# Optimization experiments

Measured on AMD Instinct MI355X. Metric: run time of the kernel, lower is better.

Reference implementation:

```python
import jax, jax.numpy as jnp
import numpy as np

SOS = 1
EOS = 2
M = 32  # max_y_seq_len


def gru_cell(x, h, W_ih, W_hh, b_ih, b_hh):
    # torch GRUCell math: gates ordered [r, z, n]
    gi = x @ W_ih.T + b_ih          # [B, 3H]
    gh = h @ W_hh.T + b_hh          # [B, 3H]
    i_r, i_z, i_n = jnp.split(gi, 3, axis=-1)
    h_r, h_z, h_n = jnp.split(gh, 3, axis=-1)
    r = jax.nn.sigmoid(i_r + h_r)
    z = jax.nn.sigmoid(i_z + h_z)
    n = jnp.tanh(i_n + r * h_n)
    return (1.0 - z) * n + z * h


def setup_inputs() -> dict:
    key = jax.random.key(0)
    ks = jax.random.split(key, 12)
    B, H, V = 256, 512, 16000
    s = 0.05  # keep GRU pre-activations in a sane range
    return {
        "sem_f": jax.random.normal(ks[0], (B, H), jnp.float32),
        "emb": jax.random.normal(ks[1], (V, H), jnp.float32) * 0.01,
        "W_ih0": jax.random.normal(ks[2], (3 * H, H), jnp.float32) * s,
        "W_hh0": jax.random.normal(ks[3], (3 * H, H), jnp.float32) * s,
        "b_ih0": jax.random.normal(ks[4], (3 * H,), jnp.float32) * s,
        "b_hh0": jax.random.normal(ks[5], (3 * H,), jnp.float32) * s,
        "W_ih1": jax.random.normal(ks[6], (3 * H, H), jnp.float32) * s,
        "W_hh1": jax.random.normal(ks[7], (3 * H, H), jnp.float32) * s,
        "b_ih1": jax.random.normal(ks[8], (3 * H,), jnp.float32) * s,
        "b_hh1": jax.random.normal(ks[9], (3 * H,), jnp.float32) * s,
        "fc_W": jax.random.normal(ks[10], (V, H), jnp.float32) * s,
        "fc_b": jax.random.normal(ks[11], (V,), jnp.float32) * s,
    }


def reference(sem_f, emb, W_ih0, W_hh0, b_ih0, b_hh0,
              W_ih1, W_hh1, b_ih1, b_hh1, fc_W, fc_b):
    B = sem_f.shape[0]
    # hidden = sem_f repeated for each GRU layer
    h0 = sem_f
    h1 = sem_f
    inputs = jnp.full((B,), SOS, dtype=jnp.int32)
    finished = jnp.zeros((B,), dtype=bool)

    def step(carry, _):
        inputs, h0, h1, finished = carry
        unf = ~finished                         # rows still active this step
        x = emb[inputs]                         # [B, H]
        h0n = gru_cell(x, h0, W_ih0, W_hh0, b_ih0, b_hh0)
        h1n = gru_cell(h0n, h1, W_ih1, W_hh1, b_ih1, b_hh1)
        out = h1n @ fc_W.T + fc_b               # [B, V]
        dec = jnp.argmax(out, axis=1).astype(jnp.int32)
        # emulate unf_idxs advanced-indexing writes: finished rows keep -1 / 0
        decoded_t = jnp.where(unf, dec, -1)
        logits_t = jnp.where(unf[:, None], out, 0.0)
        new_finished = finished | (unf & (dec == EOS))
        # pruned (finished) rows freeze hidden and inputs
        h0 = jnp.where(unf[:, None], h0n, h0)
        h1 = jnp.where(unf[:, None], h1n, h1)
        inputs = jnp.where(unf, dec, inputs)
        return (inputs, h0, h1, new_finished), (decoded_t, logits_t)

    _, (decoded, logits) = jax.lax.scan(step, (inputs, h0, h1, finished),
                                        None, length=M)
    decoded = decoded.T                          # [B, M]
    logits = jnp.transpose(logits, (1, 0, 2))    # [B, M, V]
    mask = decoded != -1
    return decoded, logits, mask
```

## Files before the change

### kernel.cpp

```cpp
#include <hip/hip_runtime.h>
#include <math.h>

#define B_   256
#define H_   512
#define V_   16000
#define M_   32
#define SOS_ 1
#define EOS_ 2
#define INV_SCALE (1.0f/2048.0f)

typedef _Float16 half_t;
typedef _Float16 f16x8 __attribute__((ext_vector_type(8)));
typedef _Float16 f16x4 __attribute__((ext_vector_type(4)));
typedef float    f32x4 __attribute__((ext_vector_type(4)));

__device__ __forceinline__ void split_f32(float x, half_t& a, half_t& b) {
    a = (half_t)x;
    b = (half_t)((x - (float)a) * 2048.0f);
}

__global__ __launch_bounds__(256)
void split_weights(const float* __restrict__ src, half_t* __restrict__ hi,
                   half_t* __restrict__ lo, int n4)
{
    const int i = blockIdx.x * 256 + threadIdx.x;
    if (i >= n4) return;
    const float4 v = ((const float4*)src)[i];
    f16x4 a, b;
    half_t t0, t1;
    split_f32(v.x, t0, t1); a[0] = t0; b[0] = t1;
    split_f32(v.y, t0, t1); a[1] = t0; b[1] = t1;
    split_f32(v.z, t0, t1); a[2] = t0; b[2] = t1;
    split_f32(v.w, t0, t1); a[3] = t0; b[3] = t1;
    ((f16x4*)hi)[i] = a;
    ((f16x4*)lo)[i] = b;
}

__global__ __launch_bounds__(256)
void init_kernel(const float* __restrict__ sem_f, const float* __restrict__ emb,
                 float* __restrict__ h0, float* __restrict__ h1,
                 half_t* __restrict__ h0a, half_t* __restrict__ h0b,
                 half_t* __restrict__ h1a, half_t* __restrict__ h1b,
                 half_t* __restrict__ xa,  half_t* __restrict__ xb,
                 int* __restrict__ inputs, int* __restrict__ finished)
{
    const int i = blockIdx.x * 256 + threadIdx.x;
    if (i < B_ * H_) {
        const float v = sem_f[i];
        h0[i] = v; h1[i] = v;
        half_t a, b; split_f32(v, a, b);
        h0a[i] = a; h0b[i] = b;
        h1a[i] = a; h1b[i] = b;
        const int j = i & (H_ - 1);
        const float xv = emb[SOS_ * H_ + j];
        half_t c, d; split_f32(xv, c, d);
        xa[i] = c; xb[i] = d;
    }
    if (i < B_) { inputs[i] = SOS_; finished[i] = 0; }
}

__global__ __launch_bounds__(256)
void gru_gemm_mfma(const half_t* __restrict__ Aia, const half_t* __restrict__ Aib,
                   const half_t* __restrict__ Aha, const half_t* __restrict__ Ahb,
                   const half_t* __restrict__ Wia, const half_t* __restrict__ Wib,
                   const half_t* __restrict__ Wha, const half_t* __restrict__ Whb,
                   const float* __restrict__ b_ih, const float* __restrict__ b_hh,
                   float* __restrict__ PRE)
{
    const int ct = blockIdx.x;
    const int rt = blockIdx.y;
    const bool is_ih = (ct < 12);
    const int wrow0 = (is_ih ? ct : ct - 12) * 128;
    const int row0  = rt * 32;
    const float*  bias = is_ih ? b_ih : b_hh;
    const half_t* Aa   = is_ih ? Aia : Aha;
    const half_t* Ab   = is_ih ? Aib : Ahb;
    const half_t* W0   = is_ih ? Wia : Wha;
    const half_t* W1   = is_ih ? Wib : Whb;

    __shared__ half_t W0s[128][40];
    __shared__ half_t W1s[128][40];

    const int tid  = threadIdx.x;
    const int w    = tid >> 6;
    const int lane = tid & 63;
    const int ll   = lane & 15;
    const int lg   = lane >> 4;

    const int sc = tid >> 1;
    const int sk = (tid & 1) * 16;
    const half_t* wp0 = W0 + (size_t)(wrow0 + sc) * H_ + sk;
    const half_t* wp1 = W1 + (size_t)(wrow0 + sc) * H_ + sk;

    f32x4 accM[2][2] = {};
    f32x4 accC[2][2] = {};

    for (int k0 = 0; k0 < H_; k0 += 32) {
        const f16x8 s0 = *(const f16x8*)(wp0 + k0);
        const f16x8 s1 = *(const f16x8*)(wp0 + k0 + 8);
        const f16x8 s2 = *(const f16x8*)(wp1 + k0);
        const f16x8 s3 = *(const f16x8*)(wp1 + k0 + 8);
        __syncthreads();
        *(f16x8*)&W0s[sc][sk]     = s0;
        *(f16x8*)&W0s[sc][sk + 8] = s1;
        *(f16x8*)&W1s[sc][sk]     = s2;
        *(f16x8*)&W1s[sc][sk + 8] = s3;
        __syncthreads();

        f16x8 a0[2], a1[2];
#pragma unroll
        for (int rf = 0; rf < 2; ++rf) {
            const size_t off = ((size_t)(row0 + 16*rf + ll) << 9) + k0 + (lg << 3);
            a0[rf] = *(const f16x8*)(Aa + off);
            a1[rf] = *(const f16x8*)(Ab + off);
        }
#pragma unroll
        for (int cf = 0; cf < 2; ++cf) {
            const int c = 32*w + 16*cf + ll;
            const f16x8 b0 = *(const f16x8*)&W0s[c][lg << 3];
            const f16x8 b1 = *(const f16x8*)&W1s[c][lg << 3];
#pragma unroll
            for (int rf = 0; rf < 2; ++rf) {
                accM[rf][cf] = __builtin_amdgcn_mfma_f32_16x16x32_f16(a0[rf], b0, accM[rf][cf], 0,0,0);
                accC[rf][cf] = __builtin_amdgcn_mfma_f32_16x16x32_f16(a0[rf], b1, accC[rf][cf], 0,0,0);
                accC[rf][cf] = __builtin_amdgcn_mfma_f32_16x16x32_f16(a1[rf], b0, accC[rf][cf], 0,0,0);
            }
        }
    }

#pragma unroll
    for (int cf = 0; cf < 2; ++cf) {
        const int cl = 32*w + 16*cf + ll;
        const float bv = bias[wrow0 + cl];
        const int c = ct * 128 + cl;
#pragma unroll
        for (int rf = 0; rf < 2; ++rf) {
#pragma unroll
            for (int r = 0; r < 4; ++r) {
                const int row = row0 + 16*rf + lg*4 + r;
                PRE[(size_t)row * 3072 + c] = accM[rf][cf][r] + accC[rf][cf][r] * INV_SCALE + bv;
            }
        }
    }
}

__global__ __launch_bounds__(256)
void gate_kernel(const float* __restrict__ PRE,
                 float* __restrict__ h,
                 half_t* __restrict__ ha, half_t* __restrict__ hb,
                 const int* __restrict__ finished)
{
    const int idx = blockIdx.x * 256 + threadIdx.x;
    const int b = idx >> 9;
    const int j = idx & 511;
    if (finished[b]) return;
    const float* p = PRE + (size_t)b * 3072;
    const float ir = p[j],        iz = p[512 + j],  in_ = p[1024 + j];
    const float hr = p[1536 + j], hz = p[2048 + j], hn  = p[2560 + j];
    const float r = 1.0f / (1.0f + expf(-(ir + hr)));
    const float z = 1.0f / (1.0f + expf(-(iz + hz)));
    const float n = tanhf(in_ + r * hn);
    const float hv = (1.0f - z) * n + z * h[idx];
    h[idx] = hv;
    half_t a, bb; split_f32(hv, a, bb);
    ha[idx] = a; hb[idx] = bb;
}

__global__ __launch_bounds__(256)
void fc_gemm_mfma(const half_t* __restrict__ Aa, const half_t* __restrict__ Ab,
                  const half_t* __restrict__ W0, const half_t* __restrict__ W1,
                  const float* __restrict__ fcb,
                  const int* __restrict__ finished,
                  float* __restrict__ logits,
                  float* __restrict__ pmax, int* __restrict__ pidx, int t)
{
    const int ct = blockIdx.x;
    const int rt = blockIdx.y;
    const int col0 = ct * 128;
    const int row0 = rt * 64;

    __shared__ half_t W0s[128][40];
    __shared__ half_t W1s[128][40];
    __shared__ float  pmS[64][2];
    __shared__ int    piS[64][2];

    const int tid  = threadIdx.x;
    const int wv   = tid >> 6;
    const int wr   = wv >> 1, wc = wv & 1;
    const int lane = tid & 63;
    const int ll   = lane & 15, lg = lane >> 4;

    const int sc = tid >> 1;
    const int sk = (tid & 1) * 16;
    const half_t* wp0 = W0 + (size_t)(col0 + sc) * H_ + sk;
    const half_t* wp1 = W1 + (size_t)(col0 + sc) * H_ + sk;

    f32x4 accM[2][4] = {};
    f32x4 accC[2][4] = {};

    for (int k0 = 0; k0 < H_; k0 += 32) {
        const f16x8 s0 = *(const f16x8*)(wp0 + k0);
        const f16x8 s1 = *(const f16x8*)(wp0 + k0 + 8);
        const f16x8 s2 = *(const f16x8*)(wp1 + k0);
        const f16x8 s3 = *(const f16x8*)(wp1 + k0 + 8);
        __syncthreads();
        *(f16x8*)&W0s[sc][sk]     = s0;
        *(f16x8*)&W0s[sc][sk + 8] = s1;
        *(f16x8*)&W1s[sc][sk]     = s2;
        *(f16x8*)&W1s[sc][sk + 8] = s3;
        __syncthreads();

        f16x8 a0[2], a1[2];
#pragma unroll
        for (int rf = 0; rf < 2; ++rf) {
            const size_t off = ((size_t)(row0 + 32*wr + 16*rf + ll) << 9) + k0 + (lg << 3);
            a0[rf] = *(const f16x8*)(Aa + off);
            a1[rf] = *(const f16x8*)(Ab + off);
        }
#pragma unroll
        for (int cf = 0; cf < 4; ++cf) {
            const int c = 64*wc + 16*cf + ll;
            const f16x8 b0 = *(const f16x8*)&W0s[c][lg << 3];
            const f16x8 b1 = *(const f16x8*)&W1s[c][lg << 3];
#pragma unroll
            for (int rf = 0; rf < 2; ++rf) {
                accM[rf][cf] = __builtin_amdgcn_mfma_f32_16x16x32_f16(a0[rf], b0, accM[rf][cf], 0,0,0);
                accC[rf][cf] = __builtin_amdgcn_mfma_f32_16x16x32_f16(a0[rf], b1, accC[rf][cf], 0,0,0);
                accC[rf][cf] = __builtin_amdgcn_mfma_f32_16x16x32_f16(a1[rf], b0, accC[rf][cf], 0,0,0);
            }
        }
    }

    int fin[2][4];
#pragma unroll
    for (int rf = 0; rf < 2; ++rf)
#pragma unroll
        for (int r = 0; r < 4; ++r)
            fin[rf][r] = finished[row0 + 32*wr + 16*rf + lg*4 + r];

    float bvv[2][4];
    int   bii[2][4];
#pragma unroll
    for (int rf = 0; rf < 2; ++rf)
#pragma unroll
        for (int r = 0; r < 4; ++r) { bvv[rf][r] = -INFINITY; bii[rf][r] = 0x7fffffff; }

#pragma unroll
    for (int cf = 0; cf < 4; ++cf) {
        const int col = col0 + 64*wc + 16*cf + ll;
        const float bv = fcb[col];
#pragma unroll
        for (int rf = 0; rf < 2; ++rf) {
#pragma unroll
            for (int r = 0; r < 4; ++r) {
                const int row = row0 + 32*wr + 16*rf + lg*4 + r;
                const float raw = accM[rf][cf][r] + accC[rf][cf][r] * INV_SCALE + bv;
                logits[((size_t)row * M_ + t) * V_ + col] = fin[rf][r] ? 0.0f : raw;
                if (raw > bvv[rf][r]) { bvv[rf][r] = raw; bii[rf][r] = col; }
            }
        }
    }

#pragma unroll
    for (int rf = 0; rf < 2; ++rf) {
#pragma unroll
        for (int r = 0; r < 4; ++r) {
            float v = bvv[rf][r]; int ix = bii[rf][r];
#pragma unroll
            for (int m = 1; m < 16; m <<= 1) {
                const float ov = __shfl_xor(v, m);
                const int   oi = __shfl_xor(ix, m);
                if (ov > v || (ov == v && oi < ix)) { v = ov; ix = oi; }
            }
            if (ll == 0) {
                const int lr = 32*wr + 16*rf + lg*4 + r;
                pmS[lr][wc] = v; piS[lr][wc] = ix;
            }
        }
    }
    __syncthreads();
    if (tid < 64) {
        float v = pmS[tid][0]; int ix = piS[tid][0];
        const float v2 = pmS[tid][1]; const int i2 = piS[tid][1];
        if (v2 > v || (v2 == v && i2 < ix)) { v = v2; ix = i2; }
        pmax[(row0 + tid) * 128 + ct] = v;
        pidx[(row0 + tid) * 128 + ct] = ix;
    }
}

__global__ __launch_bounds__(128)
void finalize_kernel(const float* __restrict__ pmax, const int* __restrict__ pidx,
                     const float* __restrict__ emb,
                     int* __restrict__ inputs, int* __restrict__ finished,
                     float* __restrict__ decoded_out, float* __restrict__ mask_out,
                     half_t* __restrict__ xa, half_t* __restrict__ xb, int t)
{
    const int b = blockIdx.x;
    const int tid = threadIdx.x;
    __shared__ float sv[128];
    __shared__ int   si[128];
    float v = -INFINITY; int ix = 0x7fffffff;
    if (tid < 125) { v = pmax[b * 128 + tid]; ix = pidx[b * 128 + tid]; }
    sv[tid] = v; si[tid] = ix;
    __syncthreads();
    for (int s = 64; s > 0; s >>= 1) {
        if (tid < s) {
            const float v2 = sv[tid + s]; const int i2 = si[tid + s];
            if (v2 > sv[tid] || (v2 == sv[tid] && i2 < si[tid])) { sv[tid] = v2; si[tid] = i2; }
        }
        __syncthreads();
    }
    __shared__ int s_tok;
    if (tid == 0) {
        const int fin = finished[b];
        const int dec = si[0];
        decoded_out[b * M_ + t] = fin ? -1.0f : (float)dec;
        mask_out   [b * M_ + t] = fin ? 0.0f : 1.0f;
        int tok;
        if (!fin) { inputs[b] = dec; if (dec == EOS_) finished[b] = 1; tok = dec; }
        else tok = inputs[b];
        s_tok = tok;
    }
    __syncthreads();
    const int tok = s_tok;
    for (int j = tid; j < H_; j += 128) {
        const float v2 = emb[(size_t)tok * H_ + j];
        half_t a, bb; split_f32(v2, a, bb);
        xa[b * H_ + j] = a; xb[b * H_ + j] = bb;
    }
}

extern "C" void kernel_launch(void* const* d_in, const int* in_sizes, int n_in,
                              void* d_out, int out_size, void* d_ws, size_t ws_size,
                              hipStream_t stream)
{
    const float* sem_f = (const float*)d_in[0];
    const float* emb   = (const float*)d_in[1];
    const float* W_ih0 = (const float*)d_in[2];
    const float* W_hh0 = (const float*)d_in[3];
    const float* b_ih0 = (const float*)d_in[4];
    const float* b_hh0 = (const float*)d_in[5];
    const float* W_ih1 = (const float*)d_in[6];
    const float* W_hh1 = (const float*)d_in[7];
    const float* b_ih1 = (const float*)d_in[8];
    const float* b_hh1 = (const float*)d_in[9];
    const float* fc_W  = (const float*)d_in[10];
    const float* fc_b  = (const float*)d_in[11];

    float* out = (float*)d_out;
    float* decoded_out = out;
    float* logits_out  = out + (size_t)B_ * M_;
    float* mask_out    = out + (size_t)B_ * M_ + (size_t)B_ * M_ * V_;

    float*  ws  = (float*)d_ws;
    float*  PRE = ws;
    float*  h0  = ws + 786432;
    float*  h1  = ws + 917504;
    half_t* h0a = (half_t*)(ws + 1048576);
    half_t* h0b = (half_t*)(ws + 1114112);
    half_t* h1a = (half_t*)(ws + 1179648);
    half_t* h1b = (half_t*)(ws + 1245184);
    half_t* xa  = (half_t*)(ws + 1310720);
    half_t* xb  = (half_t*)(ws + 1376256);
    float*  pmax = ws + 1441792;
    int*    pidx = (int*)(ws + 1474560);
    int*    inputs   = (int*)(ws + 1507328);
    int*    finished = (int*)(ws + 1507584);
    half_t* wi0a = (half_t*)(ws + 1507840);
    half_t* wi0b = (half_t*)(ws + 1901056);
    half_t* wh0a = (half_t*)(ws + 2294272);
    half_t* wh0b = (half_t*)(ws + 2687488);
    half_t* wi1a = (half_t*)(ws + 3080704);
    half_t* wi1b = (half_t*)(ws + 3473920);
    half_t* wh1a = (half_t*)(ws + 3867136);
    half_t* wh1b = (half_t*)(ws + 4260352);
    half_t* fca  = (half_t*)(ws + 4653568);
    half_t* fcbp = (half_t*)(ws + 8749568);

    const int nGru4 = (1536 * 512) / 4;
    const int nFc4  = (V_ * H_) / 4;
    split_weights<<<(nGru4 + 255) / 256, 256, 0, stream>>>(W_ih0, wi0a, wi0b, nGru4);
    split_weights<<<(nGru4 + 255) / 256, 256, 0, stream>>>(W_hh0, wh0a, wh0b, nGru4);
    split_weights<<<(nGru4 + 255) / 256, 256, 0, stream>>>(W_ih1, wi1a, wi1b, nGru4);
    split_weights<<<(nGru4 + 255) / 256, 256, 0, stream>>>(W_hh1, wh1a, wh1b, nGru4);
    split_weights<<<(nFc4 + 255) / 256, 256, 0, stream>>>(fc_W, fca, fcbp, nFc4);

    init_kernel<<<(B_ * H_ + 255) / 256, 256, 0, stream>>>(
        sem_f, emb, h0, h1, h0a, h0b, h1a, h1b, xa, xb, inputs, finished);

    const dim3 gruGrid(24, 8);
    const dim3 fcGrid(125, 4);

    for (int t = 0; t < M_; ++t) {
        gru_gemm_mfma<<<gruGrid, 256, 0, stream>>>(
            xa, xb, h0a, h0b, wi0a, wi0b, wh0a, wh0b, b_ih0, b_hh0, PRE);
        gate_kernel<<<(B_ * H_) / 256, 256, 0, stream>>>(PRE, h0, h0a, h0b, finished);
        gru_gemm_mfma<<<gruGrid, 256, 0, stream>>>(
            h0a, h0b, h1a, h1b, wi1a, wi1b, wh1a, wh1b, b_ih1, b_hh1, PRE);
        gate_kernel<<<(B_ * H_) / 256, 256, 0, stream>>>(PRE, h1, h1a, h1b, finished);
        fc_gemm_mfma<<<fcGrid, 256, 0, stream>>>(
            h1a, h1b, fca, fcbp, fc_b, finished, logits_out, pmax, pidx, t);
        finalize_kernel<<<B_, 128, 0, stream>>>(
            pmax, pidx, emb, inputs, finished, decoded_out, mask_out, xa, xb, t);
    }
}
```

Baseline: 2.979 ms.

## Fuse whole decode loop into one persistent cooperative kernel with grid syncs

Replaces the per-step chain of six kernel launches over 32 steps with a single cooperative persistent kernel. It does the weight splitting, init, both GRU layers, gates, FC and argmax finalize in one launch, separated by grid-wide barriers. GEMM tiles are also reshaped to 64 weight columns by 128 rows, so each block reuses its loaded weight tile across more batch rows. This removes launch overhead and inter-kernel gaps, at the cost of grid-sync latency and a fixed block count. A non-cooperative fallback path is kept.

```diff
diff --git a/kernel.cpp b/kernel.cpp
--- a/kernel.cpp
+++ b/kernel.cpp
@@ -1,5 +1,8 @@
 #include <hip/hip_runtime.h>
+#include <hip/hip_cooperative_groups.h>
 #include <math.h>
+
+namespace cg = cooperative_groups;
 
 #define B_   256
 #define H_   512
@@ -8,119 +11,97 @@
 #define SOS_ 1
 #define EOS_ 2
 #define INV_SCALE (1.0f/2048.0f)
+#define NTHR 256
 
 typedef _Float16 half_t;
 typedef _Float16 f16x8 __attribute__((ext_vector_type(8)));
 typedef _Float16 f16x4 __attribute__((ext_vector_type(4)));
 typedef float    f32x4 __attribute__((ext_vector_type(4)));
 
+struct Params {
+    const float *sem_f, *emb;
+    const float *b_ih0, *b_hh0, *b_ih1, *b_hh1, *fc_b;
+    const float *W_ih0, *W_hh0, *W_ih1, *W_hh1, *fc_W;
+    float *decoded, *logits, *mask;
+    float *PRE, *h0, *h1;
+    half_t *h0a, *h0b, *h1a, *h1b, *xa, *xb;
+    float *pmax; int *pidx; int *inputs; int *finished;
+    half_t *wi0a, *wi0b, *wh0a, *wh0b, *wi1a, *wi1b, *wh1a, *wh1b, *fca, *fcbp;
+};
+
 __device__ __forceinline__ void split_f32(float x, half_t& a, half_t& b) {
     a = (half_t)x;
     b = (half_t)((x - (float)a) * 2048.0f);
 }
 
-__global__ __launch_bounds__(256)
-void split_weights(const float* __restrict__ src, half_t* __restrict__ hi,
-                   half_t* __restrict__ lo, int n4)
-{
-    const int i = blockIdx.x * 256 + threadIdx.x;
-    if (i >= n4) return;
-    const float4 v = ((const float4*)src)[i];
-    f16x4 a, b;
-    half_t t0, t1;
-    split_f32(v.x, t0, t1); a[0] = t0; b[0] = t1;
-    split_f32(v.y, t0, t1); a[1] = t0; b[1] = t1;
-    split_f32(v.z, t0, t1); a[2] = t0; b[2] = t1;
-    split_f32(v.w, t0, t1); a[3] = t0; b[3] = t1;
-    ((f16x4*)hi)[i] = a;
-    ((f16x4*)lo)[i] = b;
-}
-
-__global__ __launch_bounds__(256)
-void init_kernel(const float* __restrict__ sem_f, const float* __restrict__ emb,
-                 float* __restrict__ h0, float* __restrict__ h1,
-                 half_t* __restrict__ h0a, half_t* __restrict__ h0b,
-                 half_t* __restrict__ h1a, half_t* __restrict__ h1b,
-                 half_t* __restrict__ xa,  half_t* __restrict__ xb,
-                 int* __restrict__ inputs, int* __restrict__ finished)
-{
-    const int i = blockIdx.x * 256 + threadIdx.x;
-    if (i < B_ * H_) {
-        const float v = sem_f[i];
-        h0[i] = v; h1[i] = v;
-        half_t a, b; split_f32(v, a, b);
-        h0a[i] = a; h0b[i] = b;
-        h1a[i] = a; h1b[i] = b;
-        const int j = i & (H_ - 1);
-        const float xv = emb[SOS_ * H_ + j];
-        half_t c, d; split_f32(xv, c, d);
-        xa[i] = c; xb[i] = d;
-    }
-    if (i < B_) { inputs[i] = SOS_; finished[i] = 0; }
-}
-
-__global__ __launch_bounds__(256)
-void gru_gemm_mfma(const half_t* __restrict__ Aia, const half_t* __restrict__ Aib,
-                   const half_t* __restrict__ Aha, const half_t* __restrict__ Ahb,
-                   const half_t* __restrict__ Wia, const half_t* __restrict__ Wib,
-                   const half_t* __restrict__ Wha, const half_t* __restrict__ Whb,
-                   const float* __restrict__ b_ih, const float* __restrict__ b_hh,
-                   float* __restrict__ PRE)
-{
-    const int ct = blockIdx.x;
-    const int rt = blockIdx.y;
-    const bool is_ih = (ct < 12);
-    const int wrow0 = (is_ih ? ct : ct - 12) * 128;
-    const int row0  = rt * 32;
+__device__ __forceinline__ void split_plane_dev(const float* __restrict__ src,
+    half_t* __restrict__ hi, half_t* __restrict__ lo, int n4, int gidx, int gst)
+{
+    for (int i = gidx; i < n4; i += gst) {
+        const float4 v = ((const float4*)src)[i];
+        f16x4 a, b; half_t t0, t1;
+        split_f32(v.x, t0, t1); a[0] = t0; b[0] = t1;
+        split_f32(v.y, t0, t1); a[1] = t0; b[1] = t1;
+        split_f32(v.z, t0, t1); a[2] = t0; b[2] = t1;
+        split_f32(v.w, t0, t1); a[3] = t0; b[3] = t1;
+        ((f16x4*)hi)[i] = a; ((f16x4*)lo)[i] = b;
+    }
+}
+
+
+__device__ void gru_tile(int ct, int rt,
+    const half_t* __restrict__ Aia, const half_t* __restrict__ Aib,
+    const half_t* __restrict__ Aha, const half_t* __restrict__ Ahb,
+    const half_t* __restrict__ Wia, const half_t* __restrict__ Wib,
+    const half_t* __restrict__ Wha, const half_t* __restrict__ Whb,
+    const float* __restrict__ b_ih, const float* __restrict__ b_hh,
+    float* __restrict__ PRE,
+    half_t (*W0s)[40], half_t (*W1s)[40])
+{
+    const bool is_ih = (ct < 24);
+    const int wrow0 = (is_ih ? ct : ct - 24) * 64;
+    const int row0  = rt * 128;
     const float*  bias = is_ih ? b_ih : b_hh;
-    const half_t* Aa   = is_ih ? Aia : Aha;
-    const half_t* Ab   = is_ih ? Aib : Ahb;
-    const half_t* W0   = is_ih ? Wia : Wha;
-    const half_t* W1   = is_ih ? Wib : Whb;
-
-    __shared__ half_t W0s[128][40];
-    __shared__ half_t W1s[128][40];
+    const half_t* Aa = is_ih ? Aia : Aha;
+    const half_t* Ab = is_ih ? Aib : Ahb;
+    const half_t* W0 = is_ih ? Wia : Wha;
+    const half_t* W1 = is_ih ? Wib : Whb;
 
     const int tid  = threadIdx.x;
-    const int w    = tid >> 6;
+    const int wv   = tid >> 6;
+    const int wr   = wv >> 1, wc = wv & 1;
     const int lane = tid & 63;
-    const int ll   = lane & 15;
-    const int lg   = lane >> 4;
-
-    const int sc = tid >> 1;
-    const int sk = (tid & 1) * 16;
+    const int ll   = lane & 15, lg = lane >> 4;
+    const int sc   = tid >> 2;
+    const int sk   = (tid & 3) * 8;
     const half_t* wp0 = W0 + (size_t)(wrow0 + sc) * H_ + sk;
     const half_t* wp1 = W1 + (size_t)(wrow0 + sc) * H_ + sk;
 
-    f32x4 accM[2][2] = {};
-    f32x4 accC[2][2] = {};
+    f32x4 accM[4][2] = {};
+    f32x4 accC[4][2] = {};
 
     for (int k0 = 0; k0 < H_; k0 += 32) {
         const f16x8 s0 = *(const f16x8*)(wp0 + k0);
-        const f16x8 s1 = *(const f16x8*)(wp0 + k0 + 8);
-        const f16x8 s2 = *(const f16x8*)(wp1 + k0);
-        const f16x8 s3 = *(const f16x8*)(wp1 + k0 + 8);
+        const f16x8 s1 = *(const f16x8*)(wp1 + k0);
         __syncthreads();
-        *(f16x8*)&W0s[sc][sk]     = s0;
-        *(f16x8*)&W0s[sc][sk + 8] = s1;
-        *(f16x8*)&W1s[sc][sk]     = s2;
-        *(f16x8*)&W1s[sc][sk + 8] = s3;
+        *(f16x8*)&W0s[sc][sk] = s0;
+        *(f16x8*)&W1s[sc][sk] = s1;
         __syncthreads();
 
-        f16x8 a0[2], a1[2];
-#pragma unroll
-        for (int rf = 0; rf < 2; ++rf) {
-            const size_t off = ((size_t)(row0 + 16*rf + ll) << 9) + k0 + (lg << 3);
+        f16x8 a0[4], a1[4];
+#pragma unroll
+        for (int rf = 0; rf < 4; ++rf) {
+            const size_t off = ((size_t)(row0 + 64*wr + 16*rf + ll) << 9) + k0 + (lg << 3);
             a0[rf] = *(const f16x8*)(Aa + off);
             a1[rf] = *(const f16x8*)(Ab + off);
         }
 #pragma unroll
         for (int cf = 0; cf < 2; ++cf) {
-            const int c = 32*w + 16*cf + ll;
+            const int c = 32*wc + 16*cf + ll;
             const f16x8 b0 = *(const f16x8*)&W0s[c][lg << 3];
             const f16x8 b1 = *(const f16x8*)&W1s[c][lg << 3];
 #pragma unroll
-            for (int rf = 0; rf < 2; ++rf) {
+            for (int rf = 0; rf < 4; ++rf) {
                 accM[rf][cf] = __builtin_amdgcn_mfma_f32_16x16x32_f16(a0[rf], b0, accM[rf][cf], 0,0,0);
                 accC[rf][cf] = __builtin_amdgcn_mfma_f32_16x16x32_f16(a0[rf], b1, accC[rf][cf], 0,0,0);
                 accC[rf][cf] = __builtin_amdgcn_mfma_f32_16x16x32_f16(a1[rf], b0, accC[rf][cf], 0,0,0);
@@ -130,27 +111,130 @@
 
 #pragma unroll
     for (int cf = 0; cf < 2; ++cf) {
-        const int cl = 32*w + 16*cf + ll;
+        const int cl = 32*wc + 16*cf + ll;
         const float bv = bias[wrow0 + cl];
-        const int c = ct * 128 + cl;
-#pragma unroll
-        for (int rf = 0; rf < 2; ++rf) {
+        const int c = ct * 64 + cl;
+#pragma unroll
+        for (int rf = 0; rf < 4; ++rf) {
 #pragma unroll
             for (int r = 0; r < 4; ++r) {
-                const int row = row0 + 16*rf + lg*4 + r;
+                const int row = row0 + 64*wr + 16*rf + lg*4 + r;
                 PRE[(size_t)row * 3072 + c] = accM[rf][cf][r] + accC[rf][cf][r] * INV_SCALE + bv;
             }
         }
     }
 }
 
-__global__ __launch_bounds__(256)
-void gate_kernel(const float* __restrict__ PRE,
-                 float* __restrict__ h,
-                 half_t* __restrict__ ha, half_t* __restrict__ hb,
-                 const int* __restrict__ finished)
-{
-    const int idx = blockIdx.x * 256 + threadIdx.x;
+__device__ void fc_tile(int ct, int rt,
+    const half_t* __restrict__ Aa, const half_t* __restrict__ Ab,
+    const half_t* __restrict__ W0, const half_t* __restrict__ W1,
+    const float* __restrict__ fcb, const int* __restrict__ finished,
+    float* __restrict__ logits, float* __restrict__ pmax, int* __restrict__ pidx,
+    int t, half_t (*W0s)[40], half_t (*W1s)[40], float (*pmS)[2], int (*piS)[2])
+{
+    const int col0 = ct * 64;
+    const int row0 = rt * 128;
+    const int tid  = threadIdx.x;
+    const int wv   = tid >> 6;
+    const int wr   = wv >> 1, wc = wv & 1;
+    const int lane = tid & 63;
+    const int ll   = lane & 15, lg = lane >> 4;
+    const int sc   = tid >> 2;
+    const int sk   = (tid & 3) * 8;
+    const half_t* wp0 = W0 + (size_t)(col0 + sc) * H_ + sk;
+    const half_t* wp1 = W1 + (size_t)(col0 + sc) * H_ + sk;
+
+    f32x4 accM[4][2] = {};
+    f32x4 accC[4][2] = {};
+
+    for (int k0 = 0; k0 < H_; k0 += 32) {
+        const f16x8 s0 = *(const f16x8*)(wp0 + k0);
+        const f16x8 s1 = *(const f16x8*)(wp1 + k0);
+        __syncthreads();
+        *(f16x8*)&W0s[sc][sk] = s0;
+        *(f16x8*)&W1s[sc][sk] = s1;
+        __syncthreads();
+
+        f16x8 a0[4], a1[4];
+#pragma unroll
+        for (int rf = 0; rf < 4; ++rf) {
+            const size_t off = ((size_t)(row0 + 64*wr + 16*rf + ll) << 9) + k0 + (lg << 3);
+            a0[rf] = *(const f16x8*)(Aa + off);
+            a1[rf] = *(const f16x8*)(Ab + off);
+        }
+#pragma unroll
+        for (int cf = 0; cf < 2; ++cf) {
+            const int c = 32*wc + 16*cf + ll;
+            const f16x8 b0 = *(const f16x8*)&W0s[c][lg << 3];
+            const f16x8 b1 = *(const f16x8*)&W1s[c][lg << 3];
+#pragma unroll
+            for (int rf = 0; rf < 4; ++rf) {
+                accM[rf][cf] = __builtin_amdgcn_mfma_f32_16x16x32_f16(a0[rf], b0, accM[rf][cf], 0,0,0);
+                accC[rf][cf] = __builtin_amdgcn_mfma_f32_16x16x32_f16(a0[rf], b1, accC[rf][cf], 0,0,0);
+                accC[rf][cf] = __builtin_amdgcn_mfma_f32_16x16x32_f16(a1[rf], b0, accC[rf][cf], 0,0,0);
+            }
+        }
+    }
+
+    int fin[4][4];
+    float bvv[4][4];
+    int   bii[4][4];
+#pragma unroll
+    for (int rf = 0; rf < 4; ++rf)
+#pragma unroll
+        for (int r = 0; r < 4; ++r) {
+            fin[rf][r] = finished[row0 + 64*wr + 16*rf + lg*4 + r];
+            bvv[rf][r] = -INFINITY; bii[rf][r] = 0x7fffffff;
+        }
+
+#pragma unroll
+    for (int cf = 0; cf < 2; ++cf) {
+        const int col = col0 + 32*wc + 16*cf + ll;
+        const float bv = fcb[col];
+#pragma unroll
+        for (int rf = 0; rf < 4; ++rf) {
+#pragma unroll
+            for (int r = 0; r < 4; ++r) {
+                const int row = row0 + 64*wr + 16*rf + lg*4 + r;
+                const float raw = accM[rf][cf][r] + accC[rf][cf][r] * INV_SCALE + bv;
+                logits[((size_t)row * M_ + t) * V_ + col] = fin[rf][r] ? 0.0f : raw;
+                if (raw > bvv[rf][r]) { bvv[rf][r] = raw; bii[rf][r] = col; }
+            }
+        }
+    }
+
+#pragma unroll
+    for (int rf = 0; rf < 4; ++rf) {
+#pragma unroll
+        for (int r = 0; r < 4; ++r) {
+            float v = bvv[rf][r]; int ix = bii[rf][r];
+#pragma unroll
+            for (int m = 1; m < 16; m <<= 1) {
+                const float ov = __shfl_xor(v, m);
+                const int   oi = __shfl_xor(ix, m);
+                if (ov > v || (ov == v && oi < ix)) { v = ov; ix = oi; }
+            }
+            if (ll == 0) {
+                const int lr = 64*wr + 16*rf + lg*4 + r;
+                pmS[lr][wc] = v; piS[lr][wc] = ix;
+            }
+        }
+    }
+    __syncthreads();
+    if (tid < 128) {
+        float v = pmS[tid][0]; int ix = piS[tid][0];
+        const float v2 = pmS[tid][1]; const int i2 = piS[tid][1];
+        if (v2 > v || (v2 == v && i2 < ix)) { v = v2; ix = i2; }
+        pmax[(size_t)(row0 + tid) * 256 + ct] = v;
+        pidx[(size_t)(row0 + tid) * 256 + ct] = ix;
+    }
+    __syncthreads();
+}
+
+__device__ __forceinline__ void gate_elem(const float* __restrict__ PRE,
+    float* __restrict__ h, half_t* __restrict__ ha, half_t* __restrict__ hb,
+    const int* __restrict__ finished, int idx)
+{
     const int b = idx >> 9;
     const int j = idx & 511;
     if (finished[b]) return;
@@ -166,241 +250,254 @@
     ha[idx] = a; hb[idx] = bb;
 }
 
-__global__ __launch_bounds__(256)
-void fc_gemm_mfma(const half_t* __restrict__ Aa, const half_t* __restrict__ Ab,
-                  const half_t* __restrict__ W0, const half_t* __restrict__ W1,
-                  const float* __restrict__ fcb,
-                  const int* __restrict__ finished,
-                  float* __restrict__ logits,
-                  float* __restrict__ pmax, int* __restrict__ pidx, int t)
-{
-    const int ct = blockIdx.x;
-    const int rt = blockIdx.y;
-    const int col0 = ct * 128;
-    const int row0 = rt * 64;
-
-    __shared__ half_t W0s[128][40];
-    __shared__ half_t W1s[128][40];
-    __shared__ float  pmS[64][2];
-    __shared__ int    piS[64][2];
-
-    const int tid  = threadIdx.x;
-    const int wv   = tid >> 6;
-    const int wr   = wv >> 1, wc = wv & 1;
-    const int lane = tid & 63;
-    const int ll   = lane & 15, lg = lane >> 4;
-
-    const int sc = tid >> 1;
-    const int sk = (tid & 1) * 16;
-    const half_t* wp0 = W0 + (size_t)(col0 + sc) * H_ + sk;
-    const half_t* wp1 = W1 + (size_t)(col0 + sc) * H_ + sk;
-
-    f32x4 accM[2][4] = {};
-    f32x4 accC[2][4] = {};
-
-    for (int k0 = 0; k0 < H_; k0 += 32) {
-        const f16x8 s0 = *(const f16x8*)(wp0 + k0);
-        const f16x8 s1 = *(const f16x8*)(wp0 + k0 + 8);
-        const f16x8 s2 = *(const f16x8*)(wp1 + k0);
-        const f16x8 s3 = *(const f16x8*)(wp1 + k0 + 8);
-        __syncthreads();
-        *(f16x8*)&W0s[sc][sk]     = s0;
-        *(f16x8*)&W0s[sc][sk + 8] = s1;
-        *(f16x8*)&W1s[sc][sk]     = s2;
-        *(f16x8*)&W1s[sc][sk + 8] = s3;
-        __syncthreads();
-
-        f16x8 a0[2], a1[2];
-#pragma unroll
-        for (int rf = 0; rf < 2; ++rf) {
-            const size_t off = ((size_t)(row0 + 32*wr + 16*rf + ll) << 9) + k0 + (lg << 3);
-            a0[rf] = *(const f16x8*)(Aa + off);
-            a1[rf] = *(const f16x8*)(Ab + off);
-        }
-#pragma unroll
-        for (int cf = 0; cf < 4; ++cf) {
-            const int c = 64*wc + 16*cf + ll;
-            const f16x8 b0 = *(const f16x8*)&W0s[c][lg << 3];
-            const f16x8 b1 = *(const f16x8*)&W1s[c][lg << 3];
-#pragma unroll
-            for (int rf = 0; rf < 2; ++rf) {
-                accM[rf][cf] = __builtin_amdgcn_mfma_f32_16x16x32_f16(a0[rf], b0, accM[rf][cf], 0,0,0);
-                accC[rf][cf] = __builtin_amdgcn_mfma_f32_16x16x32_f16(a0[rf], b1, accC[rf][cf], 0,0,0);
-                accC[rf][cf] = __builtin_amdgcn_mfma_f32_16x16x32_f16(a1[rf], b0, accC[rf][cf], 0,0,0);
-            }
-        }
-    }
-
-    int fin[2][4];
-#pragma unroll
-    for (int rf = 0; rf < 2; ++rf)
-#pragma unroll
-        for (int r = 0; r < 4; ++r)
-            fin[rf][r] = finished[row0 + 32*wr + 16*rf + lg*4 + r];
-
-    float bvv[2][4];
-    int   bii[2][4];
-#pragma unroll
-    for (int rf = 0; rf < 2; ++rf)
-#pragma unroll
-        for (int r = 0; r < 4; ++r) { bvv[rf][r] = -INFINITY; bii[rf][r] = 0x7fffffff; }
-
-#pragma unroll
-    for (int cf = 0; cf < 4; ++cf) {
-        const int col = col0 + 64*wc + 16*cf + ll;
-        const float bv = fcb[col];
-#pragma unroll
-        for (int rf = 0; rf < 2; ++rf) {
-#pragma unroll
-            for (int r = 0; r < 4; ++r) {
-                const int row = row0 + 32*wr + 16*rf + lg*4 + r;
-                const float raw = accM[rf][cf][r] + accC[rf][cf][r] * INV_SCALE + bv;
-                logits[((size_t)row * M_ + t) * V_ + col] = fin[rf][r] ? 0.0f : raw;
-                if (raw > bvv[rf][r]) { bvv[rf][r] = raw; bii[rf][r] = col; }
-            }
-        }
-    }
-
-#pragma unroll
-    for (int rf = 0; rf < 2; ++rf) {
-#pragma unroll
-        for (int r = 0; r < 4; ++r) {
-            float v = bvv[rf][r]; int ix = bii[rf][r];
-#pragma unroll
-            for (int m = 1; m < 16; m <<= 1) {
-                const float ov = __shfl_xor(v, m);
-                const int   oi = __shfl_xor(ix, m);
-                if (ov > v || (ov == v && oi < ix)) { v = ov; ix = oi; }
-            }
-            if (ll == 0) {
-                const int lr = 32*wr + 16*rf + lg*4 + r;
-                pmS[lr][wc] = v; piS[lr][wc] = ix;
-            }
-        }
-    }
-    __syncthreads();
-    if (tid < 64) {
-        float v = pmS[tid][0]; int ix = piS[tid][0];
-        const float v2 = pmS[tid][1]; const int i2 = piS[tid][1];
-        if (v2 > v || (v2 == v && i2 < ix)) { v = v2; ix = i2; }
-        pmax[(row0 + tid) * 128 + ct] = v;
-        pidx[(row0 + tid) * 128 + ct] = ix;
-    }
-}
-
-__global__ __launch_bounds__(128)
-void finalize_kernel(const float* __restrict__ pmax, const int* __restrict__ pidx,
-                     const float* __restrict__ emb,
-                     int* __restrict__ inputs, int* __restrict__ finished,
-                     float* __restrict__ decoded_out, float* __restrict__ mask_out,
-                     half_t* __restrict__ xa, half_t* __restrict__ xb, int t)
-{
-    const int b = blockIdx.x;
+__device__ void finalize_row(int b, const Params& p, int t,
+                             float* sv, int* si, int* s_tok)
+{
     const int tid = threadIdx.x;
-    __shared__ float sv[128];
-    __shared__ int   si[128];
     float v = -INFINITY; int ix = 0x7fffffff;
-    if (tid < 125) { v = pmax[b * 128 + tid]; ix = pidx[b * 128 + tid]; }
+    if (tid < 250) { v = p.pmax[(size_t)b * 256 + tid]; ix = p.pidx[(size_t)b * 256 + tid]; }
     sv[tid] = v; si[tid] = ix;
     __syncthreads();
-    for (int s = 64; s > 0; s >>= 1) {
+    for (int s = 128; s > 0; s >>= 1) {
         if (tid < s) {
             const float v2 = sv[tid + s]; const int i2 = si[tid + s];
             if (v2 > sv[tid] || (v2 == sv[tid] && i2 < si[tid])) { sv[tid] = v2; si[tid] = i2; }
         }
         __syncthreads();
     }
-    __shared__ int s_tok;
     if (tid == 0) {
-        const int fin = finished[b];
+        const int fin = p.finished[b];
         const int dec = si[0];
-        decoded_out[b * M_ + t] = fin ? -1.0f : (float)dec;
-        mask_out   [b * M_ + t] = fin ? 0.0f : 1.0f;
+        p.decoded[b * M_ + t] = fin ? -1.0f : (float)dec;
+        p.mask   [b * M_ + t] = fin ? 0.0f : 1.0f;
         int tok;
-        if (!fin) { inputs[b] = dec; if (dec == EOS_) finished[b] = 1; tok = dec; }
-        else tok = inputs[b];
-        s_tok = tok;
+        if (!fin) { p.inputs[b] = dec; if (dec == EOS_) p.finished[b] = 1; tok = dec; }
+        else tok = p.inputs[b];
+        *s_tok = tok;
     }
     __syncthreads();
-    const int tok = s_tok;
-    for (int j = tid; j < H_; j += 128) {
-        const float v2 = emb[(size_t)tok * H_ + j];
+    const int tok = *s_tok;
+    for (int j = tid; j < H_; j += NTHR) {
+        const float v2 = p.emb[(size_t)tok * H_ + j];
         half_t a, bb; split_f32(v2, a, bb);
-        xa[b * H_ + j] = a; xb[b * H_ + j] = bb;
-    }
+        p.xa[b * H_ + j] = a; p.xb[b * H_ + j] = bb;
+    }
+    __syncthreads();
+}
+
+__global__ __launch_bounds__(NTHR, 2)
+void scan_coop(Params p)
+{
+    cg::grid_group grid = cg::this_grid();
+
+    __shared__ half_t W0s[64][40];
+    __shared__ half_t W1s[64][40];
+    __shared__ float  red_f[256];
+    __shared__ int    red_i[256];
+    __shared__ int    s_tok;
+
+    const int nblk = gridDim.x;
+    const int blk  = blockIdx.x;
+    const int tid  = threadIdx.x;
+    const int gidx = blk * NTHR + tid;
+    const int gst  = nblk * NTHR;
+
+    split_plane_dev(p.W_ih0, p.wi0a, p.wi0b, (1536*512)/4, gidx, gst);
+    split_plane_dev(p.W_hh0, p.wh0a, p.wh0b, (1536*512)/4, gidx, gst);
+    split_plane_dev(p.W_ih1, p.wi1a, p.wi1b, (1536*512)/4, gidx, gst);
+    split_plane_dev(p.W_hh1, p.wh1a, p.wh1b, (1536*512)/4, gidx, gst);
+    split_plane_dev(p.fc_W,  p.fca,  p.fcbp, (V_*H_)/4,    gidx, gst);
+    for (int i = gidx; i < B_ * H_; i += gst) {
+        const float v = p.sem_f[i];
+        p.h0[i] = v; p.h1[i] = v;
+        half_t a, b; split_f32(v, a, b);
+        p.h0a[i] = a; p.h0b[i] = b;
+        p.h1a[i] = a; p.h1b[i] = b;
+        const int j = i & (H_ - 1);
+        const float xv = p.emb[SOS_ * H_ + j];
+        half_t c, d; split_f32(xv, c, d);
+        p.xa[i] = c; p.xb[i] = d;
+    }
+    for (int i = gidx; i < B_; i += gst) { p.inputs[i] = SOS_; p.finished[i] = 0; }
+    grid.sync();
+
+    for (int t = 0; t < M_; ++t) {
+        for (int tile = blk; tile < 96; tile += nblk)
+            gru_tile(tile % 48, tile / 48, p.xa, p.xb, p.h0a, p.h0b,
+                     p.wi0a, p.wi0b, p.wh0a, p.wh0b, p.b_ih0, p.b_hh0, p.PRE, W0s, W1s);
+        grid.sync();
+        for (int i = gidx; i < B_ * H_; i += gst)
+            gate_elem(p.PRE, p.h0, p.h0a, p.h0b, p.finished, i);
+        grid.sync();
+        for (int tile = blk; tile < 96; tile += nblk)
+            gru_tile(tile % 48, tile / 48, p.h0a, p.h0b, p.h1a, p.h1b,
+                     p.wi1a, p.wi1b, p.wh1a, p.wh1b, p.b_ih1, p.b_hh1, p.PRE, W0s, W1s);
+        grid.sync();
+        for (int i = gidx; i < B_ * H_; i += gst)
+            gate_elem(p.PRE, p.h1, p.h1a, p.h1b, p.finished, i);
+        grid.sync();
+        for (int tile = blk; tile < 500; tile += nblk)
+            fc_tile(tile % 250, tile / 250, p.h1a, p.h1b, p.fca, p.fcbp, p.fc_b,
+                    p.finished, p.logits, p.pmax, p.pidx, t, W0s, W1s,
+                    (float(*)[2])red_f, (int(*)[2])red_i);
+        grid.sync();
+        for (int b = blk; b < B_; b += nblk)
+            finalize_row(b, p, t, red_f, red_i, &s_tok);
+        grid.sync();
+    }
+}
+
+__global__ __launch_bounds__(256)
+void split_weights_k(const float* __restrict__ src, half_t* __restrict__ hi,
+                     half_t* __restrict__ lo, int n4)
+{
+    const int i = blockIdx.x * 256 + threadIdx.x;
+    if (i >= n4) return;
+    const float4 v = ((const float4*)src)[i];
+    f16x4 a, b; half_t t0, t1;
+    split_f32(v.x, t0, t1); a[0] = t0; b[0] = t1;
+    split_f32(v.y, t0, t1); a[1] = t0; b[1] = t1;
+    split_f32(v.z, t0, t1); a[2] = t0; b[2] = t1;
+    split_f32(v.w, t0, t1); a[3] = t0; b[3] = t1;
+    ((f16x4*)hi)[i] = a; ((f16x4*)lo)[i] = b;
+}
+
+__global__ __launch_bounds__(256)
+void init_k(Params p)
+{
+    const int i = blockIdx.x * 256 + threadIdx.x;
+    if (i < B_ * H_) {
+        const float v = p.sem_f[i];
+        p.h0[i] = v; p.h1[i] = v;
+        half_t a, b; split_f32(v, a, b);
+        p.h0a[i] = a; p.h0b[i] = b;
+        p.h1a[i] = a; p.h1b[i] = b;
+        const int j = i & (H_ - 1);
+        const float xv = p.emb[SOS_ * H_ + j];
+        half_t c, d; split_f32(xv, c, d);
+        p.xa[i] = c; p.xb[i] = d;
+    }
+    if (i < B_) { p.inputs[i] = SOS_; p.finished[i] = 0; }
+}
+
+__global__ __launch_bounds__(256)
+void gru_k(const half_t* Aia, const half_t* Aib, const half_t* Aha, const half_t* Ahb,
+           const half_t* Wia, const half_t* Wib, const half_t* Wha, const half_t* Whb,
+           const float* b_ih, const float* b_hh, float* PRE)
+{
+    __shared__ half_t W0s[64][40];
+    __shared__ half_t W1s[64][40];
+    gru_tile(blockIdx.x, blockIdx.y, Aia, Aib, Aha, Ahb,
+             Wia, Wib, Wha, Whb, b_ih, b_hh, PRE, W0s, W1s);
+}
+
+__global__ __launch_bounds__(256)
+void gate_k(const float* PRE, float* h, half_t* ha, half_t* hb, const int* finished)
+{
+    gate_elem(PRE, h, ha, hb, finished, blockIdx.x * 256 + threadIdx.x);
+}
+
+__global__ __launch_bounds__(256)
+void fc_k(const half_t* Aa, const half_t* Ab, const half_t* W0, const half_t* W1,
+          const float* fcb, const int* finished, float* logits,
+          float* pmax, int* pidx, int t)
+{
+    __shared__ half_t W0s[64][40];
+    __shared__ half_t W1s[64][40];
+    __shared__ float  pmS[128][2];
+    __shared__ int    piS[128][2];
+    fc_tile(blockIdx.x, blockIdx.y, Aa, Ab, W0, W1, fcb, finished,
+            logits, pmax, pidx, t, W0s, W1s, pmS, piS);
+}
+
+__global__ __launch_bounds__(256)
+void finalize_k(Params p, int t)
+{
+    __shared__ float sv[256];
+    __shared__ int   si[256];
+    __shared__ int   s_tok;
+    finalize_row(blockIdx.x, p, t, sv, si, &s_tok);
 }
 
 extern "C" void kernel_launch(void* const* d_in, const int* in_sizes, int n_in,
                               void* d_out, int out_size, void* d_ws, size_t ws_size,
                               hipStream_t stream)
 {
-    const float* sem_f = (const float*)d_in[0];
-    const float* emb   = (const float*)d_in[1];
-    const float* W_ih0 = (const float*)d_in[2];
-    const float* W_hh0 = (const float*)d_in[3];
-    const float* b_ih0 = (const float*)d_in[4];
-    const float* b_hh0 = (const float*)d_in[5];
-    const float* W_ih1 = (const float*)d_in[6];
-    const float* W_hh1 = (const float*)d_in[7];
-    const float* b_ih1 = (const float*)d_in[8];
-    const float* b_hh1 = (const float*)d_in[9];
-    const float* fc_W  = (const float*)d_in[10];
-    const float* fc_b  = (const float*)d_in[11];
+    Params p;
+    p.sem_f = (const float*)d_in[0];
+    p.emb   = (const float*)d_in[1];
+    p.W_ih0 = (const float*)d_in[2];
+    p.W_hh0 = (const float*)d_in[3];
+    p.b_ih0 = (const float*)d_in[4];
+    p.b_hh0 = (const float*)d_in[5];
+    p.W_ih1 = (const float*)d_in[6];
+    p.W_hh1 = (const float*)d_in[7];
+    p.b_ih1 = (const float*)d_in[8];
+    p.b_hh1 = (const float*)d_in[9];
+    p.fc_W  = (const float*)d_in[10];
+    p.fc_b  = (const float*)d_in[11];
 
     float* out = (float*)d_out;
-    float* decoded_out = out;
-    float* logits_out  = out + (size_t)B_ * M_;
-    float* mask_out    = out + (size_t)B_ * M_ + (size_t)B_ * M_ * V_;
-
-    float*  ws  = (float*)d_ws;
-    float*  PRE = ws;
-    float*  h0  = ws + 786432;
-    float*  h1  = ws + 917504;
-    half_t* h0a = (half_t*)(ws + 1048576);
-    half_t* h0b = (half_t*)(ws + 1114112);
-    half_t* h1a = (half_t*)(ws + 1179648);
-    half_t* h1b = (half_t*)(ws + 1245184);
-    half_t* xa  = (half_t*)(ws + 1310720);
-    half_t* xb  = (half_t*)(ws + 1376256);
-    float*  pmax = ws + 1441792;
-    int*    pidx = (int*)(ws + 1474560);
-    int*    inputs   = (int*)(ws + 1507328);
-    int*    finished = (int*)(ws + 1507584);
-    half_t* wi0a = (half_t*)(ws + 1507840);
-    half_t* wi0b = (half_t*)(ws + 1901056);
-    half_t* wh0a = (half_t*)(ws + 2294272);
-    half_t* wh0b = (half_t*)(ws + 2687488);
-    half_t* wi1a = (half_t*)(ws + 3080704);
-    half_t* wi1b = (half_t*)(ws + 3473920);
-    half_t* wh1a = (half_t*)(ws + 3867136);
-    half_t* wh1b = (half_t*)(ws + 4260352);
-    half_t* fca  = (half_t*)(ws + 4653568);
-    half_t* fcbp = (half_t*)(ws + 8749568);
+    p.decoded = out;
+    p.logits  = out + (size_t)B_ * M_;
+    p.mask    = out + (size_t)B_ * M_ + (size_t)B_ * M_ * V_;
+
+    float* ws = (float*)d_ws;
+    p.PRE  = ws;
+    p.h0   = ws + 786432;
+    p.h1   = ws + 917504;
+    p.h0a  = (half_t*)(ws + 1048576);
+    p.h0b  = (half_t*)(ws + 1114112);
+    p.h1a  = (half_t*)(ws + 1179648);
+    p.h1b  = (half_t*)(ws + 1245184);
+    p.xa   = (half_t*)(ws + 1310720);
+    p.xb   = (half_t*)(ws + 1376256);
+    p.pmax = ws + 1441792;
+    p.pidx = (int*)(ws + 1507328);
+    p.inputs   = (int*)(ws + 1572864);
+    p.finished = (int*)(ws + 1573120);
+    p.wi0a = (half_t*)(ws + 1573376);
+    p.wi0b = (half_t*)(ws + 1966592);
+    p.wh0a = (half_t*)(ws + 2359808);
+    p.wh0b = (half_t*)(ws + 2753024);
+    p.wi1a = (half_t*)(ws + 3146240);
+    p.wi1b = (half_t*)(ws + 3539456);
+    p.wh1a = (half_t*)(ws + 3932672);
+    p.wh1b = (half_t*)(ws + 4325888);
+    p.fca  = (half_t*)(ws + 4719104);
+    p.fcbp = (half_t*)(ws + 8815104);
+
+    int occ = 0;
+    hipError_t oe = hipOccupancyMaxActiveBlocksPerMultiprocessor(&occ, scan_coop, NTHR, 0);
+    hipError_t le = hipErrorUnknown;
+    if (oe == hipSuccess && occ >= 1) {
+        const int nblk = (occ >= 2) ? 512 : 256;
+        void* args[] = { &p };
+        le = hipLaunchCooperativeKernel((const void*)scan_coop, dim3(nblk), dim3(NTHR),
+                                        args, 0, stream);
+    }
+    if (le == hipSuccess) return;
 
     const int nGru4 = (1536 * 512) / 4;
     const int nFc4  = (V_ * H_) / 4;
-    split_weights<<<(nGru4 + 255) / 256, 256, 0, stream>>>(W_ih0, wi0a, wi0b, nGru4);
-    split_weights<<<(nGru4 + 255) / 256, 256, 0, stream>>>(W_hh0, wh0a, wh0b, nGru4);
-    split_weights<<<(nGru4 + 255) / 256, 256, 0, stream>>>(W_ih1, wi1a, wi1b, nGru4);
-    split_weights<<<(nGru4 + 255) / 256, 256, 0, stream>>>(W_hh1, wh1a, wh1b, nGru4);
-    split_weights<<<(nFc4 + 255) / 256, 256, 0, stream>>>(fc_W, fca, fcbp, nFc4);
-
-    init_kernel<<<(B_ * H_ + 255) / 256, 256, 0, stream>>>(
-        sem_f, emb, h0, h1, h0a, h0b, h1a, h1b, xa, xb, inputs, finished);
-
-    const dim3 gruGrid(24, 8);
-    const dim3 fcGrid(125, 4);
-
+    split_weights_k<<<(nGru4 + 255) / 256, 256, 0, stream>>>(p.W_ih0, p.wi0a, p.wi0b, nGru4);
+    split_weights_k<<<(nGru4 + 255) / 256, 256, 0, stream>>>(p.W_hh0, p.wh0a, p.wh0b, nGru4);
+    split_weights_k<<<(nGru4 + 255) / 256, 256, 0, stream>>>(p.W_ih1, p.wi1a, p.wi1b, nGru4);
+    split_weights_k<<<(nGru4 + 255) / 256, 256, 0, stream>>>(p.W_hh1, p.wh1a, p.wh1b, nGru4);
+    split_weights_k<<<(nFc4 + 255) / 256, 256, 0, stream>>>(p.fc_W, p.fca, p.fcbp, nFc4);
+    init_k<<<(B_ * H_ + 255) / 256, 256, 0, stream>>>(p);
+
+    const dim3 gruGrid(48, 2);
+    const dim3 fcGrid(250, 2);
     for (int t = 0; t < M_; ++t) {
-        gru_gemm_mfma<<<gruGrid, 256, 0, stream>>>(
-            xa, xb, h0a, h0b, wi0a, wi0b, wh0a, wh0b, b_ih0, b_hh0, PRE);
-        gate_kernel<<<(B_ * H_) / 256, 256, 0, stream>>>(PRE, h0, h0a, h0b, finished);
-        gru_gemm_mfma<<<gruGrid, 256, 0, stream>>>(
-            h0a, h0b, h1a, h1b, wi1a, wi1b, wh1a, wh1b, b_ih1, b_hh1, PRE);
-        gate_kernel<<<(B_ * H_) / 256, 256, 0, stream>>>(PRE, h1, h1a, h1b, finished);
-        fc_gemm_mfma<<<fcGrid, 256, 0, stream>>>(
-            h1a, h1b, fca, fcbp, fc_b, finished, logits_out, pmax, pidx, t);
-        finalize_kernel<<<B_, 128, 0, stream>>>(
-            pmax, pidx, emb, inputs, finished, decoded_out, mask_out, xa, xb, t);
-    }
-}
+        gru_k<<<gruGrid, 256, 0, stream>>>(p.xa, p.xb, p.h0a, p.h0b,
+            p.wi0a, p.wi0b, p.wh0a, p.wh0b, p.b_ih0, p.b_hh0, p.PRE);
+        gate_k<<<(B_ * H_) / 256, 256, 0, stream>>>(p.PRE, p.h0, p.h0a, p.h0b, p.finished);
+        gru_k<<<gruGrid, 256, 0, stream>>>(p.h0a, p.h0b, p.h1a, p.h1b,
+            p.wi1a, p.wi1b, p.wh1a, p.wh1b, p.b_ih1, p.b_hh1, p.PRE);
+        gate_k<<<(B_ * H_) / 256, 256, 0, stream>>>(p.PRE, p.h1, p.h1a, p.h1b, p.finished);
+        fc_k<<<fcGrid, 256, 0, stream>>>(p.h1a, p.h1b, p.fca, p.fcbp, p.fc_b,
+            p.finished, p.logits, p.pmax, p.pidx, t);
+        finalize_k<<<B_, 256, 0, stream>>>(p, t);
+    }
+}
```

After: 4.024 ms, median of 4. 1.35x slower.
